# Optimization experiments

Hardware: AMD Instinct MI355X
Metric: run time of the kernel (lower is better)

The kernel has to match this reference:

```python
import jax, jax.numpy as jnp
import numpy as np
from jax import lax

D_MODEL = 1024
N_EXPERTS = 8
N_ACTIVE = 2
FFN_HIDDEN = int(D_MODEL * 2.0)


def setup_inputs() -> dict:
    key = jax.random.key(0)
    ks = jax.random.split(key, 7)
    B, T = 2, 2048
    s_in = 1.0 / np.sqrt(D_MODEL)
    s_h = 1.0 / np.sqrt(FFN_HIDDEN)
    return {
        "x": jax.random.normal(ks[0], (B, T, D_MODEL), dtype=jnp.float32),
        # router: torch Linear(d_model, n_experts, bias=False) weight [E, D]
        "router_w": jax.random.uniform(ks[1], (N_EXPERTS, D_MODEL), jnp.float32, -s_in, s_in),
        # stacked expert FFN params: w1 [E, H, D], b1 [E, H], w2 [E, D, H], b2 [E, D]
        "w1": jax.random.uniform(ks[2], (N_EXPERTS, FFN_HIDDEN, D_MODEL), jnp.float32, -s_in, s_in),
        "b1": jax.random.uniform(ks[3], (N_EXPERTS, FFN_HIDDEN), jnp.float32, -s_in, s_in),
        "w2": jax.random.uniform(ks[4], (N_EXPERTS, D_MODEL, FFN_HIDDEN), jnp.float32, -s_h, s_h),
        "b2": jax.random.uniform(ks[5], (N_EXPERTS, D_MODEL), jnp.float32, -s_h, s_h),
    }


def reference(x, router_w, w1, b1, w2, b2):
    B, T, D = x.shape
    N = B * T
    xf = x.reshape(N, D)

    logits = xf @ router_w.T                      # [N, E]
    probs = jax.nn.softmax(logits, axis=-1)       # [N, E]

    # --- aux load-balancing loss (f_i is non-differentiable, from indices) ---
    _, disp_idx = lax.top_k(logits, N_ACTIVE)     # [N, K]
    disp_mask = jax.nn.one_hot(disp_idx, N_EXPERTS, dtype=logits.dtype).sum(axis=1)  # [N, E]
    f_i = disp_mask.sum(axis=0) / (N * N_ACTIVE)  # [E]
    P_i = probs.mean(axis=0)                      # [E]
    aux_loss = N_EXPERTS * jnp.sum(f_i * P_i)

    # --- top-k combine weights, renormalized ---
    topk_w, topk_idx = lax.top_k(probs, N_ACTIVE)                 # [N, K]
    topk_w = topk_w / topk_w.sum(axis=-1, keepdims=True)
    # scatter top-k weights into dense [N, E] combine matrix (zeros elsewhere)
    combine_w = (jax.nn.one_hot(topk_idx, N_EXPERTS, dtype=xf.dtype) * topk_w[..., None]).sum(axis=1)

    # --- expert FFNs, weighted combine (loop over small fixed expert set) ---
    out = jnp.zeros_like(xf)
    for e in range(N_EXPERTS):
        h = jax.nn.silu(xf @ w1[e].T + b1[e])     # [N, H]
        y = h @ w2[e].T + b2[e]                   # [N, D]
        out = out + combine_w[:, e:e + 1] * y

    return out.reshape(B, T, D), aux_loss
```

## Files before the change

kernel.cpp:

```cpp
#include <hip/hip_runtime.h>
#include <cstdint>
#include <cstddef>

#define D_MODEL 1024
#define N_EXPERTS 8
#define FFN_H 2048
#define N_TOK 4096
#define CAP 2048

typedef float f32x4 __attribute__((ext_vector_type(4)));
typedef __bf16 bf16x8 __attribute__((ext_vector_type(8)));

static constexpr size_t XB_OFF   = 0;
static constexpr size_t W1B_OFF  = XB_OFF  + (size_t)N_TOK * D_MODEL * 2;
static constexpr size_t W2B_OFF  = W1B_OFF + (size_t)N_EXPERTS * FFN_H * D_MODEL * 2;
static constexpr size_t HBUF_OFF = W2B_OFF + (size_t)N_EXPERTS * D_MODEL * FFN_H * 2;
static constexpr size_t YBUF_OFF = HBUF_OFF + (size_t)N_EXPERTS * CAP * FFN_H * 2;
static constexpr size_t CNT_OFF  = YBUF_OFF + (size_t)N_EXPERTS * CAP * D_MODEL * 2;
static constexpr size_t PSUM_OFF = CNT_OFF + 32;
static constexpr size_t TOK_OFF  = PSUM_OFF + 32;
static constexpr size_t TIX_OFF  = TOK_OFF + (size_t)N_EXPERTS * CAP * 4;
static constexpr size_t TIW_OFF  = TIX_OFF + (size_t)N_TOK * 8;

__device__ __forceinline__ void async_ld16(const void* g, void* l) {
    __builtin_amdgcn_global_load_lds(
        (const __attribute__((address_space(1))) unsigned int*)g,
        (__attribute__((address_space(3))) unsigned int*)l, 16, 0, 0);
}

__device__ __forceinline__ void cvt_block(const float* __restrict__ src,
                                          __bf16* __restrict__ dst,
                                          int c, int tid) {
    size_t i = (size_t)c * 2048 + (size_t)tid * 8;
    float4 a = *reinterpret_cast<const float4*>(src + i);
    float4 d = *reinterpret_cast<const float4*>(src + i + 4);
    bf16x8 r;
    r[0] = (__bf16)a.x; r[1] = (__bf16)a.y; r[2] = (__bf16)a.z; r[3] = (__bf16)a.w;
    r[4] = (__bf16)d.x; r[5] = (__bf16)d.y; r[6] = (__bf16)d.z; r[7] = (__bf16)d.w;
    *reinterpret_cast<bf16x8*>(dst + i) = r;
}

__global__ __launch_bounds__(256) void prep_kernel(const float* __restrict__ x,
                                                   const float* __restrict__ rw,
                                                   const float* __restrict__ w1,
                                                   __bf16* __restrict__ xb,
                                                   __bf16* __restrict__ w1b,
                                                   int* __restrict__ counts,
                                                   float* __restrict__ psum,
                                                   int* __restrict__ tok_list,
                                                   int2* __restrict__ tinfo_idx,
                                                   float2* __restrict__ tinfo_w) {
    __shared__ float rws[N_EXPERTS * D_MODEL];
    __shared__ int s_e0[64], s_e1[64], s_r0[64], s_r1[64];
    __shared__ float s_w0[64], s_w1[64];
    __shared__ int hist[8], base[8];
    __shared__ float pacc[8];

    int tid = threadIdx.x;
    int b = blockIdx.x;
    if (b >= 64) {
        int c = b - 64;
        if (c < 2048) cvt_block(x, xb, c, tid);
        else          cvt_block(w1, w1b, c - 2048, tid);
        return;
    }

    for (int i = tid * 4; i < N_EXPERTS * D_MODEL; i += 256 * 4)
        *reinterpret_cast<float4*>(&rws[i]) = *reinterpret_cast<const float4*>(&rw[i]);
    if (tid < 8) { hist[tid] = 0; pacc[tid] = 0.f; }
    __syncthreads();

    int wave = tid >> 6, lane = tid & 63;
    float psacc[8] = {};
    for (int it = 0; it < 16; ++it) {
        int li = wave * 16 + it;
        int t = b * 64 + li;
        const float* xr = x + (size_t)t * D_MODEL;
        float acc[8] = {};
#pragma unroll
        for (int i = 0; i < D_MODEL / 64; ++i) {
            float xv = xr[lane + 64 * i];
#pragma unroll
            for (int e = 0; e < 8; ++e) acc[e] += xv * rws[e * D_MODEL + lane + 64 * i];
        }
        float logit[8];
#pragma unroll
        for (int e = 0; e < 8; ++e) {
            float v = acc[e];
            for (int off = 32; off; off >>= 1) v += __shfl_xor(v, off);
            logit[e] = v;
        }
        float mx = logit[0];
#pragma unroll
        for (int e = 1; e < 8; ++e) mx = fmaxf(mx, logit[e]);
        float p[8], s = 0.f;
#pragma unroll
        for (int e = 0; e < 8; ++e) { p[e] = expf(logit[e] - mx); s += p[e]; }
        float inv = 1.f / s;
#pragma unroll
        for (int e = 0; e < 8; ++e) { p[e] *= inv; psacc[e] += p[e]; }
        int e0 = 0; float p0 = p[0];
#pragma unroll
        for (int e = 1; e < 8; ++e) if (p[e] > p0) { p0 = p[e]; e0 = e; }
        int e1 = -1; float p1 = -1.f;
#pragma unroll
        for (int e = 0; e < 8; ++e) if (e != e0 && p[e] > p1) { p1 = p[e]; e1 = e; }
        float invw = 1.f / (p0 + p1);
        if (lane == 0) {
            s_e0[li] = e0; s_e1[li] = e1;
            s_w0[li] = p0 * invw; s_w1[li] = p1 * invw;
        }
    }
    if (lane == 0)
#pragma unroll
        for (int e = 0; e < 8; ++e) atomicAdd(&pacc[e], psacc[e]);
    __syncthreads();

    if (tid < 64) {
        s_r0[tid] = atomicAdd(&hist[s_e0[tid]], 1);
        s_r1[tid] = atomicAdd(&hist[s_e1[tid]], 1);
    }
    __syncthreads();
    if (tid < 8) {
        base[tid] = atomicAdd(&counts[tid], hist[tid]);
        atomicAdd(&psum[tid], pacc[tid]);
    }
    __syncthreads();
    if (tid < 64) {
        int t = b * 64 + tid;
        int e0 = s_e0[tid], e1 = s_e1[tid];
        int q0 = min(base[e0] + s_r0[tid], CAP - 1);
        int q1 = min(base[e1] + s_r1[tid], CAP - 1);
        tok_list[e0 * CAP + q0] = t;
        tok_list[e1 * CAP + q1] = t;
        tinfo_idx[t] = make_int2(e0 * CAP + q0, e1 * CAP + q1);
        tinfo_w[t] = make_float2(s_w0[tid], s_w1[tid]);
    }
}

template <int KDIM, bool PASS2, bool CVT>
__global__ __launch_bounds__(256, 4) void ffn_kernel(const __bf16* __restrict__ A_base,
                                                     const __bf16* __restrict__ B_base,
                                                     const float* __restrict__ bias,
                                                     const int* __restrict__ counts,
                                                     const int* __restrict__ tok_list,
                                                     __bf16* __restrict__ Out_base,
                                                     const float* __restrict__ cvt_src,
                                                     __bf16* __restrict__ cvt_dst) {
    constexpr int BROWS = PASS2 ? D_MODEL : FFN_H;
    constexpr int NT = BROWS / 128;
    constexpr int NSTEP = KDIM / 32;
    int bid = blockIdx.x;
    int tid = threadIdx.x;

    int gid;
    if (CVT) {
        int m5 = bid % 5;
        if (m5) {
            cvt_block(cvt_src, cvt_dst, (bid / 5) * 4 + m5 - 1, tid);
            return;
        }
        gid = bid / 5;
    } else {
        gid = bid;
    }

    int e = gid & 7;
    int r = gid >> 3;
    int n0 = (r % NT) * 128;
    int m0 = (r / NT) * 128;
    int cnt = min(counts[e], CAP);
    if (m0 >= cnt) return;

    __shared__ char smem[36864];

    int* s_tok = (int*)smem;
    if (!PASS2 && tid < 128) {
        int slot = min(m0 + tid, cnt - 1);
        s_tok[tid] = tok_list[e * CAP + slot];
    }
    __syncthreads();

    int colk = ((tid & 3) ^ ((tid >> 3) & 3)) * 8;
    const __bf16 *a_src0, *a_src1;
    if (PASS2) {
        int s0 = min(m0 + (tid >> 2), cnt - 1);
        int s1 = min(m0 + 64 + (tid >> 2), cnt - 1);
        a_src0 = A_base + ((size_t)e * CAP + s0) * KDIM + colk;
        a_src1 = A_base + ((size_t)e * CAP + s1) * KDIM + colk;
    } else {
        a_src0 = A_base + (size_t)s_tok[tid >> 2] * KDIM + colk;
        a_src1 = A_base + (size_t)s_tok[64 + (tid >> 2)] * KDIM + colk;
    }
    const __bf16* b_src0 = B_base + ((size_t)e * BROWS + n0 + (tid >> 2)) * KDIM + colk;
    const __bf16* b_src1 = b_src0 + (size_t)64 * KDIM;
    __syncthreads();

    int wv = tid >> 6, lane = tid & 63;
    int wm = wv >> 1, wn = wv & 1;
    int lm = lane & 15, q = lane >> 4;
    int rsw = (q ^ ((lm >> 1) & 3)) * 8;
    int a_base = (wm * 64 + lm) * 32 + rsw;
    int b_base = (wn * 64 + lm) * 32 + rsw;
    int wofs = wv * 1024;

    f32x4 acc[4][4] = {};

    auto stage = [&](int t) {
        int k0 = t * 32;
        int bo = (t & 1) * 8192;
        char* la = smem + bo + wofs;
        char* lb = smem + 16384 + bo + wofs;
        async_ld16(a_src0 + k0, la);
        async_ld16(a_src1 + k0, la + 4096);
        async_ld16(b_src0 + k0, lb);
        async_ld16(b_src1 + k0, lb + 4096);
    };
    auto compute = [&](int t) {
        int bo = (t & 1) * 8192;
        const __bf16* pa = (const __bf16*)(smem + bo);
        const __bf16* pb = (const __bf16*)(smem + 16384 + bo);
        bf16x8 af[4], bfg[4];
#pragma unroll
        for (int f = 0; f < 4; ++f) {
            af[f]  = *reinterpret_cast<const bf16x8*>(&pa[a_base + f * 512]);
            bfg[f] = *reinterpret_cast<const bf16x8*>(&pb[b_base + f * 512]);
        }
#pragma unroll
        for (int fm = 0; fm < 4; ++fm)
#pragma unroll
            for (int fn = 0; fn < 4; ++fn)
                acc[fm][fn] = __builtin_amdgcn_mfma_f32_16x16x32_bf16(af[fm], bfg[fn], acc[fm][fn], 0, 0, 0);
    };

    stage(0);
    __syncthreads();
    for (int t = 0; t < NSTEP; ++t) {
        if (t + 1 < NSTEP) stage(t + 1);
        compute(t);
        __syncthreads();
    }

    __bf16* ep = (__bf16*)(smem) + wv * (64 * 72);
#pragma unroll
    for (int fn = 0; fn < 4; ++fn) {
        int n = n0 + wn * 64 + fn * 16 + lm;
        float bv = bias[e * BROWS + n];
#pragma unroll
        for (int fm = 0; fm < 4; ++fm)
#pragma unroll
            for (int i = 0; i < 4; ++i) {
                float v = acc[fm][fn][i] + bv;
                if (!PASS2) v = v / (1.f + __expf(-v));
                ep[(fm * 16 + q * 4 + i) * 72 + fn * 16 + lm] = (__bf16)v;
            }
    }
    __syncthreads();
    int rr = lane >> 3, ccol = (lane & 7) * 8;
#pragma unroll
    for (int rep = 0; rep < 8; ++rep) {
        int rw = rep * 8 + rr;
        int slot = m0 + wm * 64 + rw;
        bf16x8 vv = *reinterpret_cast<const bf16x8*>(&ep[rw * 72 + ccol]);
        if (slot < cnt)
            *reinterpret_cast<bf16x8*>(
                &Out_base[((size_t)e * CAP + slot) * BROWS + n0 + wn * 64 + ccol]) = vv;
    }
}

__global__ __launch_bounds__(256) void combine_kernel(const __bf16* __restrict__ ybuf,
                                                      const int2* __restrict__ tinfo_idx,
                                                      const float2* __restrict__ tinfo_w,
                                                      const int* __restrict__ counts,
                                                      const float* __restrict__ psum,
                                                      float* __restrict__ out) {
    int tid = threadIdx.x;
    if (blockIdx.x == 0 && tid == 0) {
        float s = 0.f;
#pragma unroll
        for (int e = 0; e < 8; ++e)
            s += ((float)counts[e] / (float)(N_TOK * 2)) * (psum[e] / (float)N_TOK);
        out[(size_t)N_TOK * D_MODEL] = 8.f * s;
    }
    int t = blockIdx.x * 2 + (tid >> 7);
    int d0 = (tid & 127) * 8;
    int2 ix = tinfo_idx[t];
    float2 w = tinfo_w[t];
    bf16x8 ya = *reinterpret_cast<const bf16x8*>(ybuf + (size_t)ix.x * D_MODEL + d0);
    bf16x8 yb = *reinterpret_cast<const bf16x8*>(ybuf + (size_t)ix.y * D_MODEL + d0);
    float4 o0, o1;
    o0.x = w.x * (float)ya[0] + w.y * (float)yb[0];
    o0.y = w.x * (float)ya[1] + w.y * (float)yb[1];
    o0.z = w.x * (float)ya[2] + w.y * (float)yb[2];
    o0.w = w.x * (float)ya[3] + w.y * (float)yb[3];
    o1.x = w.x * (float)ya[4] + w.y * (float)yb[4];
    o1.y = w.x * (float)ya[5] + w.y * (float)yb[5];
    o1.z = w.x * (float)ya[6] + w.y * (float)yb[6];
    o1.w = w.x * (float)ya[7] + w.y * (float)yb[7];
    float* op = out + (size_t)t * D_MODEL + d0;
    *reinterpret_cast<float4*>(op) = o0;
    *reinterpret_cast<float4*>(op + 4) = o1;
}

extern "C" void kernel_launch(void* const* d_in, const int* in_sizes, int n_in,
                              void* d_out, int out_size, void* d_ws, size_t ws_size,
                              hipStream_t stream) {
    const float* x  = (const float*)d_in[0];
    const float* rw = (const float*)d_in[1];
    const float* w1 = (const float*)d_in[2];
    const float* b1 = (const float*)d_in[3];
    const float* w2 = (const float*)d_in[4];
    const float* b2 = (const float*)d_in[5];
    float* out = (float*)d_out;

    char* ws = (char*)d_ws;
    __bf16* xb     = (__bf16*)(ws + XB_OFF);
    __bf16* w1b    = (__bf16*)(ws + W1B_OFF);
    __bf16* w2b    = (__bf16*)(ws + W2B_OFF);
    __bf16* hbuf   = (__bf16*)(ws + HBUF_OFF);
    __bf16* ybuf   = (__bf16*)(ws + YBUF_OFF);
    int*    counts = (int*)(ws + CNT_OFF);
    float*  psum   = (float*)(ws + PSUM_OFF);
    int*    tok    = (int*)(ws + TOK_OFF);
    int2*   tix    = (int2*)(ws + TIX_OFF);
    float2* tiw    = (float2*)(ws + TIW_OFF);

    hipMemsetAsync(ws + CNT_OFF, 0, 64, stream);

    prep_kernel<<<64 + 2048 + 8192, 256, 0, stream>>>(x, rw, w1, xb, w1b,
                                                      counts, psum, tok, tix, tiw);

    constexpr int NG1 = 8 * (FFN_H / 128) * (CAP / 128);
    ffn_kernel<D_MODEL, false, true><<<NG1 + 8192, 256, 0, stream>>>(
        xb, w1b, b1, counts, tok, hbuf, w2, w2b);

    constexpr int NG2 = 8 * (D_MODEL / 128) * (CAP / 128);
    ffn_kernel<FFN_H, true, false><<<NG2, 256, 0, stream>>>(
        hbuf, w2b, b2, counts, tok, ybuf, nullptr, nullptr);

    combine_kernel<<<N_TOK / 2, 256, 0, stream>>>(ybuf, tix, tiw, counts, psum, out);
}
```

Before: 283.9 us.

## Restructure expert GEMMs into 256x128 tiles with three-stage LDS pipeline

The expert FFN GEMM kernel moves from 256-thread blocks with 128x128 tiles and a double-buffered K=32 loop to 512-thread blocks with 256x128 tiles. It now uses a triple-buffered K=64 loop with split load phases, explicit vmcnt waits, raw barriers and MFMA priority hints. The fused weight-conversion blocks are resized to match the new block size. The goal is more reuse of each B tile, deeper overlap of global-to-LDS copies with MFMA work, and fewer barrier stalls. The cost is one block per CU using about 147KB of LDS, so there is less latency hiding across blocks and more wasted work on partially filled 256-row tiles.

```diff
diff --git a/kernel.cpp b/kernel.cpp
--- a/kernel.cpp
+++ b/kernel.cpp
@@ -28,9 +28,12 @@
         (__attribute__((address_space(3))) unsigned int*)l, 16, 0, 0);
 }
 
-__device__ __forceinline__ void cvt_block(const float* __restrict__ src,
-                                          __bf16* __restrict__ dst,
-                                          int c, int tid) {
+#define VMWAIT(n) asm volatile("s_waitcnt vmcnt(" #n ")" ::: "memory")
+#define SBAR()    asm volatile("s_barrier" ::: "memory")
+
+__device__ __forceinline__ void cvt_block256(const float* __restrict__ src,
+                                             __bf16* __restrict__ dst,
+                                             int c, int tid) {
     size_t i = (size_t)c * 2048 + (size_t)tid * 8;
     float4 a = *reinterpret_cast<const float4*>(src + i);
     float4 d = *reinterpret_cast<const float4*>(src + i + 4);
@@ -60,8 +63,8 @@
     int b = blockIdx.x;
     if (b >= 64) {
         int c = b - 64;
-        if (c < 2048) cvt_block(x, xb, c, tid);
-        else          cvt_block(w1, w1b, c - 2048, tid);
+        if (c < 2048) cvt_block256(x, xb, c, tid);
+        else          cvt_block256(w1, w1b, c - 2048, tid);
         return;
     }
 
@@ -139,7 +142,7 @@
 }
 
 template <int KDIM, bool PASS2, bool CVT>
-__global__ __launch_bounds__(256, 4) void ffn_kernel(const __bf16* __restrict__ A_base,
+__global__ __launch_bounds__(512, 1) void ffn_kernel(const __bf16* __restrict__ A_base,
                                                      const __bf16* __restrict__ B_base,
                                                      const float* __restrict__ bias,
                                                      const int* __restrict__ counts,
@@ -149,7 +152,7 @@
                                                      __bf16* __restrict__ cvt_dst) {
     constexpr int BROWS = PASS2 ? D_MODEL : FFN_H;
     constexpr int NT = BROWS / 128;
-    constexpr int NSTEP = KDIM / 32;
+    constexpr int NTILE = KDIM / 64;
     int bid = blockIdx.x;
     int tid = threadIdx.x;
 
@@ -157,7 +160,14 @@
     if (CVT) {
         int m5 = bid % 5;
         if (m5) {
-            cvt_block(cvt_src, cvt_dst, (bid / 5) * 4 + m5 - 1, tid);
+            int c = (bid / 5) * 4 + m5 - 1;
+            size_t i = (size_t)c * 4096 + (size_t)tid * 8;
+            float4 a = *reinterpret_cast<const float4*>(cvt_src + i);
+            float4 d = *reinterpret_cast<const float4*>(cvt_src + i + 4);
+            bf16x8 rr_;
+            rr_[0] = (__bf16)a.x; rr_[1] = (__bf16)a.y; rr_[2] = (__bf16)a.z; rr_[3] = (__bf16)a.w;
+            rr_[4] = (__bf16)d.x; rr_[5] = (__bf16)d.y; rr_[6] = (__bf16)d.z; rr_[7] = (__bf16)d.w;
+            *reinterpret_cast<bf16x8*>(cvt_dst + i) = rr_;
             return;
         }
         gid = bid / 5;
@@ -168,89 +178,146 @@
     int e = gid & 7;
     int r = gid >> 3;
     int n0 = (r % NT) * 128;
-    int m0 = (r / NT) * 128;
+    int m0 = (r / NT) * 256;
     int cnt = min(counts[e], CAP);
     if (m0 >= cnt) return;
 
-    __shared__ char smem[36864];
-
-    int* s_tok = (int*)smem;
-    if (!PASS2 && tid < 128) {
-        int slot = min(m0 + tid, cnt - 1);
-        s_tok[tid] = tok_list[e * CAP + slot];
-    }
-    __syncthreads();
-
-    int colk = ((tid & 3) ^ ((tid >> 3) & 3)) * 8;
-    const __bf16 *a_src0, *a_src1;
-    if (PASS2) {
-        int s0 = min(m0 + (tid >> 2), cnt - 1);
-        int s1 = min(m0 + 64 + (tid >> 2), cnt - 1);
-        a_src0 = A_base + ((size_t)e * CAP + s0) * KDIM + colk;
-        a_src1 = A_base + ((size_t)e * CAP + s1) * KDIM + colk;
+    __shared__ char smem[147456];
+
+    int w = tid >> 6, lane = tid & 63;
+    int sub = (tid >> 3) & 7;
+    int cbs = ((tid & 7) ^ sub) * 8;
+
+    const __bf16* a_src[4];
+    const __bf16* b_src[2];
+    if (!PASS2) {
+        int* s_tok = (int*)smem;
+        if (tid < 256) s_tok[tid] = tok_list[e * CAP + min(m0 + tid, cnt - 1)];
+        __syncthreads();
+#pragma unroll
+        for (int l = 0; l < 4; ++l)
+            a_src[l] = A_base + (size_t)s_tok[64 * l + 8 * w + sub] * KDIM + cbs;
+        __syncthreads();
     } else {
-        a_src0 = A_base + (size_t)s_tok[tid >> 2] * KDIM + colk;
-        a_src1 = A_base + (size_t)s_tok[64 + (tid >> 2)] * KDIM + colk;
-    }
-    const __bf16* b_src0 = B_base + ((size_t)e * BROWS + n0 + (tid >> 2)) * KDIM + colk;
-    const __bf16* b_src1 = b_src0 + (size_t)64 * KDIM;
-    __syncthreads();
-
-    int wv = tid >> 6, lane = tid & 63;
-    int wm = wv >> 1, wn = wv & 1;
+#pragma unroll
+        for (int l = 0; l < 4; ++l)
+            a_src[l] = A_base + ((size_t)e * CAP + min(m0 + 64 * l + 8 * w + sub, cnt - 1)) * KDIM + cbs;
+    }
+#pragma unroll
+    for (int l = 0; l < 2; ++l)
+        b_src[l] = B_base + ((size_t)e * BROWS + n0 + 64 * l + 8 * w + sub) * KDIM + cbs;
+
+    int wm = w >> 1, wn = w & 1;
     int lm = lane & 15, q = lane >> 4;
-    int rsw = (q ^ ((lm >> 1) & 3)) * 8;
-    int a_base = (wm * 64 + lm) * 32 + rsw;
-    int b_base = (wn * 64 + lm) * 32 + rsw;
-    int wofs = wv * 1024;
+    int sw0 = (q ^ (lm & 7)) * 16;
+    int sw1 = ((4 + q) ^ (lm & 7)) * 16;
+    int a_rb = (wm * 64 + lm) * 128;
+    int b_rb = 32768 + (wn * 64 + lm) * 128;
+
+    auto stage_ph0 = [&](int t) {
+        char* sb_ = smem + (t % 3) * 49152;
+        async_ld16(a_src[0] + t * 64, sb_ + (0 * 8 + w) * 1024);
+        async_ld16(a_src[1] + t * 64, sb_ + (1 * 8 + w) * 1024);
+        async_ld16(b_src[0] + t * 64, sb_ + 32768 + (0 * 8 + w) * 1024);
+    };
+    auto stage_ph1 = [&](int t) {
+        char* sb_ = smem + (t % 3) * 49152;
+        async_ld16(a_src[2] + t * 64, sb_ + (2 * 8 + w) * 1024);
+        async_ld16(a_src[3] + t * 64, sb_ + (3 * 8 + w) * 1024);
+        async_ld16(b_src[1] + t * 64, sb_ + 32768 + (1 * 8 + w) * 1024);
+    };
 
     f32x4 acc[4][4] = {};
-
-    auto stage = [&](int t) {
-        int k0 = t * 32;
-        int bo = (t & 1) * 8192;
-        char* la = smem + bo + wofs;
-        char* lb = smem + 16384 + bo + wofs;
-        async_ld16(a_src0 + k0, la);
-        async_ld16(a_src1 + k0, la + 4096);
-        async_ld16(b_src0 + k0, lb);
-        async_ld16(b_src1 + k0, lb + 4096);
-    };
-    auto compute = [&](int t) {
-        int bo = (t & 1) * 8192;
-        const __bf16* pa = (const __bf16*)(smem + bo);
-        const __bf16* pb = (const __bf16*)(smem + 16384 + bo);
-        bf16x8 af[4], bfg[4];
-#pragma unroll
-        for (int f = 0; f < 4; ++f) {
-            af[f]  = *reinterpret_cast<const bf16x8*>(&pa[a_base + f * 512]);
-            bfg[f] = *reinterpret_cast<const bf16x8*>(&pb[b_base + f * 512]);
-        }
+    bf16x8 bfr0, bfr1, bfr2, bfr3, bfs0, bfs1, bfs2, bfs3;
+
+    stage_ph0(0); stage_ph1(0); stage_ph0(1); stage_ph1(1);
+    VMWAIT(6);
+    SBAR();
+
+    for (int t = 0; t < NTILE; ++t) {
+        const char* sb_ = smem + (t % 3) * 49152;
+        if (t + 2 < NTILE) stage_ph0(t + 2);
+        bf16x8 a00, a01, a10, a11;
+        bfr0 = *reinterpret_cast<const bf16x8*>(sb_ + b_rb + 0 * 2048 + sw0);
+        bfs0 = *reinterpret_cast<const bf16x8*>(sb_ + b_rb + 0 * 2048 + sw1);
+        bfr1 = *reinterpret_cast<const bf16x8*>(sb_ + b_rb + 1 * 2048 + sw0);
+        bfs1 = *reinterpret_cast<const bf16x8*>(sb_ + b_rb + 1 * 2048 + sw1);
+        bfr2 = *reinterpret_cast<const bf16x8*>(sb_ + b_rb + 2 * 2048 + sw0);
+        bfs2 = *reinterpret_cast<const bf16x8*>(sb_ + b_rb + 2 * 2048 + sw1);
+        bfr3 = *reinterpret_cast<const bf16x8*>(sb_ + b_rb + 3 * 2048 + sw0);
+        bfs3 = *reinterpret_cast<const bf16x8*>(sb_ + b_rb + 3 * 2048 + sw1);
+        a00 = *reinterpret_cast<const bf16x8*>(sb_ + a_rb + 0 * 2048 + sw0);
+        a01 = *reinterpret_cast<const bf16x8*>(sb_ + a_rb + 0 * 2048 + sw1);
+        a10 = *reinterpret_cast<const bf16x8*>(sb_ + a_rb + 1 * 2048 + sw0);
+        a11 = *reinterpret_cast<const bf16x8*>(sb_ + a_rb + 1 * 2048 + sw1);
+        SBAR();
+        asm volatile("s_waitcnt lgkmcnt(0)" ::: "memory");
+        __builtin_amdgcn_sched_barrier(0);
+        __builtin_amdgcn_s_setprio(1);
+        acc[0][0] = __builtin_amdgcn_mfma_f32_16x16x32_bf16(a00, bfr0, acc[0][0], 0, 0, 0);
+        acc[0][1] = __builtin_amdgcn_mfma_f32_16x16x32_bf16(a00, bfr1, acc[0][1], 0, 0, 0);
+        acc[0][2] = __builtin_amdgcn_mfma_f32_16x16x32_bf16(a00, bfr2, acc[0][2], 0, 0, 0);
+        acc[0][3] = __builtin_amdgcn_mfma_f32_16x16x32_bf16(a00, bfr3, acc[0][3], 0, 0, 0);
+        acc[1][0] = __builtin_amdgcn_mfma_f32_16x16x32_bf16(a10, bfr0, acc[1][0], 0, 0, 0);
+        acc[1][1] = __builtin_amdgcn_mfma_f32_16x16x32_bf16(a10, bfr1, acc[1][1], 0, 0, 0);
+        acc[1][2] = __builtin_amdgcn_mfma_f32_16x16x32_bf16(a10, bfr2, acc[1][2], 0, 0, 0);
+        acc[1][3] = __builtin_amdgcn_mfma_f32_16x16x32_bf16(a10, bfr3, acc[1][3], 0, 0, 0);
+        acc[0][0] = __builtin_amdgcn_mfma_f32_16x16x32_bf16(a01, bfs0, acc[0][0], 0, 0, 0);
+        acc[0][1] = __builtin_amdgcn_mfma_f32_16x16x32_bf16(a01, bfs1, acc[0][1], 0, 0, 0);
+        acc[0][2] = __builtin_amdgcn_mfma_f32_16x16x32_bf16(a01, bfs2, acc[0][2], 0, 0, 0);
+        acc[0][3] = __builtin_amdgcn_mfma_f32_16x16x32_bf16(a01, bfs3, acc[0][3], 0, 0, 0);
+        acc[1][0] = __builtin_amdgcn_mfma_f32_16x16x32_bf16(a11, bfs0, acc[1][0], 0, 0, 0);
+        acc[1][1] = __builtin_amdgcn_mfma_f32_16x16x32_bf16(a11, bfs1, acc[1][1], 0, 0, 0);
+        acc[1][2] = __builtin_amdgcn_mfma_f32_16x16x32_bf16(a11, bfs2, acc[1][2], 0, 0, 0);
+        acc[1][3] = __builtin_amdgcn_mfma_f32_16x16x32_bf16(a11, bfs3, acc[1][3], 0, 0, 0);
+        __builtin_amdgcn_s_setprio(0);
+        SBAR();
+        if (t + 2 < NTILE) stage_ph1(t + 2);
+        bf16x8 a20, a21, a30, a31;
+        a20 = *reinterpret_cast<const bf16x8*>(sb_ + a_rb + 2 * 2048 + sw0);
+        a21 = *reinterpret_cast<const bf16x8*>(sb_ + a_rb + 2 * 2048 + sw1);
+        a30 = *reinterpret_cast<const bf16x8*>(sb_ + a_rb + 3 * 2048 + sw0);
+        a31 = *reinterpret_cast<const bf16x8*>(sb_ + a_rb + 3 * 2048 + sw1);
+        SBAR();
+        asm volatile("s_waitcnt lgkmcnt(0)" ::: "memory");
+        __builtin_amdgcn_sched_barrier(0);
+        __builtin_amdgcn_s_setprio(1);
+        acc[2][0] = __builtin_amdgcn_mfma_f32_16x16x32_bf16(a20, bfr0, acc[2][0], 0, 0, 0);
+        acc[2][1] = __builtin_amdgcn_mfma_f32_16x16x32_bf16(a20, bfr1, acc[2][1], 0, 0, 0);
+        acc[2][2] = __builtin_amdgcn_mfma_f32_16x16x32_bf16(a20, bfr2, acc[2][2], 0, 0, 0);
+        acc[2][3] = __builtin_amdgcn_mfma_f32_16x16x32_bf16(a20, bfr3, acc[2][3], 0, 0, 0);
+        acc[3][0] = __builtin_amdgcn_mfma_f32_16x16x32_bf16(a30, bfr0, acc[3][0], 0, 0, 0);
+        acc[3][1] = __builtin_amdgcn_mfma_f32_16x16x32_bf16(a30, bfr1, acc[3][1], 0, 0, 0);
+        acc[3][2] = __builtin_amdgcn_mfma_f32_16x16x32_bf16(a30, bfr2, acc[3][2], 0, 0, 0);
+        acc[3][3] = __builtin_amdgcn_mfma_f32_16x16x32_bf16(a30, bfr3, acc[3][3], 0, 0, 0);
+        acc[2][0] = __builtin_amdgcn_mfma_f32_16x16x32_bf16(a21, bfs0, acc[2][0], 0, 0, 0);
+        acc[2][1] = __builtin_amdgcn_mfma_f32_16x16x32_bf16(a21, bfs1, acc[2][1], 0, 0, 0);
+        acc[2][2] = __builtin_amdgcn_mfma_f32_16x16x32_bf16(a21, bfs2, acc[2][2], 0, 0, 0);
+        acc[2][3] = __builtin_amdgcn_mfma_f32_16x16x32_bf16(a21, bfs3, acc[2][3], 0, 0, 0);
+        acc[3][0] = __builtin_amdgcn_mfma_f32_16x16x32_bf16(a31, bfs0, acc[3][0], 0, 0, 0);
+        acc[3][1] = __builtin_amdgcn_mfma_f32_16x16x32_bf16(a31, bfs1, acc[3][1], 0, 0, 0);
+        acc[3][2] = __builtin_amdgcn_mfma_f32_16x16x32_bf16(a31, bfs2, acc[3][2], 0, 0, 0);
+        acc[3][3] = __builtin_amdgcn_mfma_f32_16x16x32_bf16(a31, bfs3, acc[3][3], 0, 0, 0);
+        __builtin_amdgcn_s_setprio(0);
+        if (t < NTILE - 2)       VMWAIT(6);
+        else if (t == NTILE - 2) VMWAIT(0);
+        SBAR();
+    }
+
+    float bv[4];
+    {
+        int nb = e * BROWS + n0 + wn * 64 + lm;
+#pragma unroll
+        for (int fn = 0; fn < 4; ++fn) bv[fn] = bias[nb + fn * 16];
+    }
+    __bf16* ep = (__bf16*)(smem) + w * (64 * 72);
+#pragma unroll
+    for (int fn = 0; fn < 4; ++fn) {
 #pragma unroll
         for (int fm = 0; fm < 4; ++fm)
 #pragma unroll
-            for (int fn = 0; fn < 4; ++fn)
-                acc[fm][fn] = __builtin_amdgcn_mfma_f32_16x16x32_bf16(af[fm], bfg[fn], acc[fm][fn], 0, 0, 0);
-    };
-
-    stage(0);
-    __syncthreads();
-    for (int t = 0; t < NSTEP; ++t) {
-        if (t + 1 < NSTEP) stage(t + 1);
-        compute(t);
-        __syncthreads();
-    }
-
-    __bf16* ep = (__bf16*)(smem) + wv * (64 * 72);
-#pragma unroll
-    for (int fn = 0; fn < 4; ++fn) {
-        int n = n0 + wn * 64 + fn * 16 + lm;
-        float bv = bias[e * BROWS + n];
-#pragma unroll
-        for (int fm = 0; fm < 4; ++fm)
-#pragma unroll
             for (int i = 0; i < 4; ++i) {
-                float v = acc[fm][fn][i] + bv;
+                float v = acc[fm][fn][i] + bv[fn];
                 if (!PASS2) v = v / (1.f + __expf(-v));
                 ep[(fm * 16 + q * 4 + i) * 72 + fn * 16 + lm] = (__bf16)v;
             }
@@ -330,12 +397,12 @@
     prep_kernel<<<64 + 2048 + 8192, 256, 0, stream>>>(x, rw, w1, xb, w1b,
                                                       counts, psum, tok, tix, tiw);
 
-    constexpr int NG1 = 8 * (FFN_H / 128) * (CAP / 128);
-    ffn_kernel<D_MODEL, false, true><<<NG1 + 8192, 256, 0, stream>>>(
+    constexpr int NG1 = 8 * (FFN_H / 128) * (CAP / 256);
+    ffn_kernel<D_MODEL, false, true><<<NG1 * 5, 512, 0, stream>>>(
         xb, w1b, b1, counts, tok, hbuf, w2, w2b);
 
-    constexpr int NG2 = 8 * (D_MODEL / 128) * (CAP / 128);
-    ffn_kernel<FFN_H, true, false><<<NG2, 256, 0, stream>>>(
+    constexpr int NG2 = 8 * (D_MODEL / 128) * (CAP / 256);
+    ffn_kernel<FFN_H, true, false><<<NG2, 512, 0, stream>>>(
         hbuf, w2b, b2, counts, tok, ybuf, nullptr, nullptr);
 
     combine_kernel<<<N_TOK / 2, 256, 0, stream>>>(ybuf, tix, tiw, counts, psum, out);
```

New measurement: 314.2 us. 1.11x slower.
